# Performance work log

Hardware: AMD Instinct MI355X
Metric: run time of the kernel (lower is better)

## Reference

```python
import jax, jax.numpy as jnp
import numpy as np

NEG_SLOPE = 0.2


def setup_inputs() -> dict:
    key = jax.random.key(0)
    k1, k2, k3, k4, k5, k6 = jax.random.split(key, 6)
    N, E, IN, OUT = 100000, 1600000, 256, 32
    feat = jax.random.normal(k1, (N, IN), dtype=jnp.float32)
    W = jax.random.normal(k2, (IN, OUT), dtype=jnp.float32) * (1.0 / np.sqrt(IN))
    attn_l = jax.random.normal(k3, (OUT,), dtype=jnp.float32) * 0.1
    attn_r = jax.random.normal(k4, (OUT,), dtype=jnp.float32) * 0.1
    bias = jnp.zeros((OUT,), dtype=jnp.float32)
    src = jax.random.randint(k5, (E,), 0, N, dtype=jnp.int32)
    dst = jax.random.randint(k6, (E,), 0, N, dtype=jnp.int32)
    return {"feat": feat, "W": W, "attn_l": attn_l, "attn_r": attn_r,
            "bias": bias, "src": src, "dst": dst}


def reference(feat, W, attn_l, attn_r, bias, src, dst):
    N = feat.shape[0]
    # dense projection: [N, in] @ [in, out] -> [N, out]
    h = feat @ W
    el = h @ attn_l  # [N]
    er = h @ attn_r  # [N]
    # per-edge raw score: el[u] + er[v] for edge u->v
    e = el[src] + er[dst]  # [E]
    e = jnp.where(e > 0, e, NEG_SLOPE * e)  # leaky relu
    # edge softmax grouped by destination node (numerically stable)
    m = jax.ops.segment_max(e, dst, num_segments=N)  # [N], -inf for isolated nodes
    m = jax.lax.stop_gradient(m)
    ex = jnp.exp(e - m[dst])  # [E]
    denom = jax.ops.segment_sum(ex, dst, num_segments=N)  # [N]
    alpha = ex / denom[dst]  # [E]
    # weighted aggregation (sparse SpMM): sum_{u->v} alpha_uv * h[u]
    rst = jax.ops.segment_sum(h[src] * alpha[:, None], dst, num_segments=N)  # [N, out]
    return rst + bias
```

## Files before the change

kernel.cpp:

```cpp
#include <hip/hip_runtime.h>
#include <hip/hip_bf16.h>
#include <math.h>

#define NEG_SLOPE 0.2f
#define BUCK_BITS 5
#define BUCK_NODES 32
#define CAP 800
#define SRC_MASK 0x1FFFFFF
#define NBUK_MAX 3200

#define CBITS 8
#define CNODES 256
#define CAPC 4672
#define NC_MAX 400
#define NBIN 256

typedef __bf16 bf16x8 __attribute__((ext_vector_type(8)));
typedef __bf16 bf16x4 __attribute__((ext_vector_type(4)));
typedef float  f32x4  __attribute__((ext_vector_type(4)));

__global__ void prep(const float* __restrict__ W, __bf16* __restrict__ Whi,
                     unsigned int* __restrict__ fcur,
                     unsigned int* __restrict__ ccur) {
    int idx = blockIdx.x * blockDim.x + threadIdx.x;
    if (idx < NBUK_MAX) fcur[idx] = 0u;
    if (idx < NC_MAX)   ccur[idx] = 0u;
    if (idx >= 8192) return;
    int j = idx & 7, lane = (idx >> 3) & 63, nt = (idx >> 9) & 1, kt = idx >> 10;
    int q = lane >> 4, c = lane & 15;
    int k = kt * 32 + q * 8 + j;
    int n = nt * 16 + c;
    Whi[idx] = (__bf16)W[k * 32 + n];
}

__global__ __launch_bounds__(256) void gemm_bin(const float* __restrict__ feat,
                                                const __bf16* __restrict__ Whi,
                                                const float* __restrict__ attn_l,
                                                const float* __restrict__ attn_r,
                                                const int* __restrict__ src,
                                                const int* __restrict__ dst,
                                                __bf16* __restrict__ hb,
                                                float* __restrict__ el,
                                                float* __restrict__ er,
                                                unsigned int* __restrict__ ccur,
                                                unsigned int* __restrict__ cbin,
                                                int N, int Ntiles, int E, int NC) {
    __shared__ bf16x8 sB[1024];
    int bid = blockIdx.x;
    int tid = threadIdx.x;
    int role, gid;
    if (bid < 2 * NBIN) { role = bid & 1; gid = bid >> 1; }
    else                { role = 0;       gid = bid - NBIN; }

    if (role == 1) {
        unsigned int* hist  = (unsigned int*)sB;
        unsigned int* cbase = hist + NC_MAX;
        int batch = (((E + NBIN - 1) / NBIN) + 3) & ~3;
        int b0 = gid * batch;
        int b1 = min(b0 + batch, E);
        int nv = (b0 < b1) ? ((b1 - b0) >> 2) : 0;
        const int4* d4 = (const int4*)(dst + b0);
        const int4* s4 = (const int4*)(src + b0);
        for (int i = tid; i < NC; i += 256) hist[i] = 0;
        __syncthreads();
        for (int i = tid; i < nv; i += 256) {
            int4 dd = d4[i];
#pragma unroll
            for (int j = 0; j < 4; j++)
                atomicAdd(&hist[((unsigned)(&dd.x)[j]) >> CBITS], 1u);
        }
        __syncthreads();
        for (int i = tid; i < NC; i += 256) {
            unsigned c = hist[i];
            cbase[i] = c ? atomicAdd(&ccur[i], c) : 0u;
            hist[i] = 0;
        }
        __syncthreads();
        for (int i = tid; i < nv; i += 256) {
            int4 dd = d4[i];
            int4 ss = s4[i];
#pragma unroll
            for (int j = 0; j < 4; j++) {
                int d = (&dd.x)[j];
                int s = (&ss.x)[j];
                unsigned cb = ((unsigned)d) >> CBITS;
                unsigned r = atomicAdd(&hist[cb], 1u);
                unsigned pos = cbase[cb] + r;
                if (pos < CAPC)
                    cbin[(size_t)cb * CAPC + pos] =
                        ((unsigned)(d & (CNODES - 1)) << 17) | (unsigned)s;
            }
        }
        return;
    }

    for (int i = tid; i < 1024; i += 256) sB[i] = ((const bf16x8*)Whi)[i];
    __syncthreads();

    int wid  = gid * 4 + (tid >> 6);
    int lane = tid & 63;
    if (wid >= Ntiles) return;

    int c = lane & 15, q = lane >> 4;
    int row = wid * 16 + c;
    if (row >= N) row = N - 1;
    const f32x4* A = (const f32x4*)(feat + (size_t)row * 256 + q * 8);

    f32x4 a[16];
#pragma unroll
    for (int kt = 0; kt < 8; kt++) {
        a[2 * kt]     = A[kt * 8];
        a[2 * kt + 1] = A[kt * 8 + 1];
    }
#pragma unroll
    for (int i = 0; i < 16; i++)
        asm volatile("" : "+v"(a[i]));
    __builtin_amdgcn_sched_barrier(0);

    f32x4 acc0 = {0.f, 0.f, 0.f, 0.f};
    f32x4 acc1 = {0.f, 0.f, 0.f, 0.f};
#pragma unroll
    for (int kt = 0; kt < 8; kt++) {
        f32x4 a0 = a[2 * kt];
        f32x4 a1 = a[2 * kt + 1];
        bf16x8 ah, al;
#pragma unroll
        for (int j = 0; j < 4; j++) {
            __bf16 h0 = (__bf16)a0[j];
            __bf16 h1 = (__bf16)a1[j];
            ah[j]     = h0;
            ah[j + 4] = h1;
            al[j]     = (__bf16)(a0[j] - (float)h0);
            al[j + 4] = (__bf16)(a1[j] - (float)h1);
        }
        bf16x8 bh0 = sB[(kt * 2 + 0) * 64 + lane];
        bf16x8 bh1 = sB[(kt * 2 + 1) * 64 + lane];
        acc0 = __builtin_amdgcn_mfma_f32_16x16x32_bf16(ah, bh0, acc0, 0, 0, 0);
        acc0 = __builtin_amdgcn_mfma_f32_16x16x32_bf16(al, bh0, acc0, 0, 0, 0);
        acc1 = __builtin_amdgcn_mfma_f32_16x16x32_bf16(ah, bh1, acc1, 0, 0, 0);
        acc1 = __builtin_amdgcn_mfma_f32_16x16x32_bf16(al, bh1, acc1, 0, 0, 0);
    }

    float alc  = attn_l[c],      arc  = attn_r[c];
    float alc2 = attn_l[c + 16], arc2 = attn_r[c + 16];
#pragma unroll
    for (int r = 0; r < 4; r++) {
        int m = wid * 16 + q * 4 + r;
        if (m < N) {
            hb[(size_t)m * 32 + c]      = (__bf16)acc0[r];
            hb[(size_t)m * 32 + 16 + c] = (__bf16)acc1[r];
        }
        float pl = acc0[r] * alc + acc1[r] * alc2;
        float pr = acc0[r] * arc + acc1[r] * arc2;
#pragma unroll
        for (int off = 8; off >= 1; off >>= 1) {
            pl += __shfl_xor(pl, off);
            pr += __shfl_xor(pr, off);
        }
        if (c == 0 && m < N) { el[m] = pl; er[m] = pr; }
    }
}

__global__ __launch_bounds__(256) void refine(const unsigned int* __restrict__ ccur,
                                              const unsigned int* __restrict__ cbin,
                                              unsigned int* __restrict__ fcur,
                                              unsigned int* __restrict__ fbin,
                                              int NC) {
    __shared__ unsigned int hist[8];
    __shared__ unsigned int basec[8];
    int blk = blockIdx.x;
    int cb = blk >> 1, seg = blk & 1;
    if (cb >= NC) return;
    int tid = threadIdx.x;
    int cnt = (int)min(ccur[cb], (unsigned)CAPC);
    int lo = (cnt * seg) >> 1;
    int hi = (cnt * (seg + 1)) >> 1;

    if (tid < 8) hist[tid] = 0;
    __syncthreads();
    const unsigned int* cp = cbin + (size_t)cb * CAPC;
    for (int i = lo + tid; i < hi; i += 256)
        atomicAdd(&hist[(cp[i] >> (17 + BUCK_BITS)) & 7], 1u);
    __syncthreads();
    if (tid < 8) {
        unsigned v = hist[tid];
        basec[tid] = v ? atomicAdd(&fcur[cb * 8 + tid], v) : 0u;
        hist[tid] = 0;
    }
    __syncthreads();
    for (int i = lo + tid; i < hi; i += 256) {
        unsigned r = cp[i];
        int fb = (r >> (17 + BUCK_BITS)) & 7;
        unsigned rank = atomicAdd(&hist[fb], 1u);
        unsigned pos = basec[fb] + rank;
        if (pos < CAP)
            fbin[(size_t)(cb * 8 + fb) * CAP + pos] =
                (((r >> 17) & (BUCK_NODES - 1)) << 25) | (r & 0x1FFFFu);
    }
}

__global__ __launch_bounds__(256) void aggregate(const unsigned int* __restrict__ cursor,
                                                 const unsigned int* __restrict__ binned,
                                                 const float* __restrict__ el,
                                                 const float* __restrict__ er,
                                                 const __bf16* __restrict__ hb,
                                                 const float* __restrict__ bias,
                                                 float* __restrict__ out, int N) {
    __shared__ uint2        rw_s[CAP];
    __shared__ unsigned int hist[BUCK_NODES];
    __shared__ int          off_s[BUCK_NODES + 1];
    __shared__ float        den[BUCK_NODES];
    __shared__ float        er_l[BUCK_NODES];

    int buck = blockIdx.x;
    int base = buck << BUCK_BITS;
    int nn = min(BUCK_NODES, N - base);
    int tid = threadIdx.x;

    int cnt = (int)min(cursor[buck], (unsigned)CAP);
    const unsigned int* eb = binned + (size_t)buck * CAP;

    if (tid < BUCK_NODES) {
        hist[tid] = 0;
        den[tid] = 0.f;
        er_l[tid] = (tid < nn) ? er[base + tid] : 0.f;
    }
    __syncthreads();

    unsigned int rl[4];
    int k = 0;
    for (int i = tid; i < cnt; i += 256) {
        unsigned r = eb[i];
        rl[k++] = r;
        atomicAdd(&hist[r >> 25], 1u);
    }
    __syncthreads();

    if (tid < BUCK_NODES) {
        int v = (int)hist[tid];
        int orig = v;
#pragma unroll
        for (int off = 1; off < BUCK_NODES; off <<= 1) {
            int x = __shfl_up(v, off, 64);
            if (tid >= off) v += x;
        }
        off_s[tid] = v - orig;
        if (tid == BUCK_NODES - 1) off_s[BUCK_NODES] = v;
        hist[tid] = (unsigned)(v - orig);
    }
    __syncthreads();

    k = 0;
    for (int i = tid; i < cnt; i += 256) {
        unsigned r = rl[k++];
        int s = r & SRC_MASK;
        int d = r >> 25;
        float e = el[s] + er_l[d];
        e = (e > 0.f) ? e : NEG_SLOPE * e;
        float w = __expf(e);
        unsigned pos = atomicAdd(&hist[d], 1u);
        rw_s[pos] = make_uint2((unsigned)s, __float_as_uint(w));
        atomicAdd(&den[d], w);
    }
    __syncthreads();

    int lane = tid & 63, wv = tid >> 6;
    int oct = lane >> 3, t = lane & 7;
    f32x4 b4 = *(const f32x4*)&bias[t * 4];
    for (int n = wv; n < nn; n += 4) {
        float sm = den[n];
        int s0 = off_s[n], s1 = off_s[n + 1];
        f32x4 acc = {0.f, 0.f, 0.f, 0.f};
#pragma unroll 2
        for (int j = s0 + oct; j < s1; j += 8) {
            uint2 rw = rw_s[j];
            float w = __uint_as_float(rw.y);
            bf16x4 hv = *(const bf16x4*)&hb[(size_t)rw.x * 32 + t * 4];
            acc[0] += w * (float)hv[0];
            acc[1] += w * (float)hv[1];
            acc[2] += w * (float)hv[2];
            acc[3] += w * (float)hv[3];
        }
#pragma unroll
        for (int off = 8; off <= 32; off <<= 1) {
            acc[0] += __shfl_xor(acc[0], off);
            acc[1] += __shfl_xor(acc[1], off);
            acc[2] += __shfl_xor(acc[2], off);
            acc[3] += __shfl_xor(acc[3], off);
        }
        if (lane < 8) {
            f32x4 o;
            if (sm > 0.f) {
                float inv = 1.f / sm;
                o[0] = acc[0] * inv + b4[0];
                o[1] = acc[1] * inv + b4[1];
                o[2] = acc[2] * inv + b4[2];
                o[3] = acc[3] * inv + b4[3];
            } else {
                o = b4;
            }
            *(f32x4*)&out[(size_t)(base + n) * 32 + t * 4] = o;
        }
    }
}

static inline size_t align256(size_t x) { return (x + 255) & ~(size_t)255; }

extern "C" void kernel_launch(void* const* d_in, const int* in_sizes, int n_in,
                              void* d_out, int out_size, void* d_ws, size_t ws_size,
                              hipStream_t stream) {
    const float* feat   = (const float*)d_in[0];
    const float* W      = (const float*)d_in[1];
    const float* attn_l = (const float*)d_in[2];
    const float* attn_r = (const float*)d_in[3];
    const float* bias   = (const float*)d_in[4];
    const int* src = (const int*)d_in[5];
    const int* dst = (const int*)d_in[6];
    float* out = (float*)d_out;

    const int IN = 256;
    int N = in_sizes[0] / IN;
    int E = in_sizes[5];
    (void)n_in; (void)out_size; (void)ws_size;

    int Ntiles = (N + 15) / 16;
    int NBUK = (N + BUCK_NODES - 1) >> BUCK_BITS;
    int NC   = (N + CNODES - 1) >> CBITS;
    int NG   = (Ntiles + 3) / 4;

    char* p = (char*)d_ws;
    __bf16* hb     = (__bf16*)p; p += align256((size_t)N * 32 * 2);
    float* el      = (float*)p; p += align256((size_t)N * 4);
    float* er      = (float*)p; p += align256((size_t)N * 4);
    unsigned int* fcur = (unsigned int*)p; p += align256((size_t)NBUK_MAX * 4);
    unsigned int* ccur = (unsigned int*)p; p += align256((size_t)NC_MAX * 4);
    unsigned int* fbin = (unsigned int*)p; p += align256((size_t)NBUK * CAP * 4);
    unsigned int* cbin = (unsigned int*)p; p += align256((size_t)NC * CAPC * 4);
    __bf16* Whi    = (__bf16*)p; p += align256((size_t)8192 * 2);

    prep<<<33, 256, 0, stream>>>(W, Whi, fcur, ccur);
    gemm_bin<<<NG + NBIN, 256, 0, stream>>>(feat, Whi, attn_l, attn_r, src, dst,
                                            hb, el, er, ccur, cbin,
                                            N, Ntiles, E, NC);
    refine<<<NC * 2, 256, 0, stream>>>(ccur, cbin, fcur, fbin, NC);
    aggregate<<<NBUK, 256, 0, stream>>>(fcur, fbin, el, er, hb, bias, out, N);
}
```

Measured before the change: 249.0 us.

## Make GEMM blocks persistent with double-buffered async global-to-LDS feature staging

Replaces the one-tile-per-wave GEMM launch with 256 persistent GEMM blocks interleaved with the 256 binning blocks. Each wave loops over tiles strided by 1024. Feature rows are streamed into a per-wave double-buffered, XOR-swizzled LDS stage using global_load_lds, with explicit vmcnt waits, so the next quarter-tile loads while the current one runs on MFMA. The aim is to hide the latency of the feature load, which is bound by memory bandwidth. In exchange it uses much more LDS per block (16 KB of weights plus 32 KB of staging), which may lower occupancy. It also relies on the hand-tuned waitcnt being correct.

```diff
diff --git a/kernel.cpp b/kernel.cpp
--- a/kernel.cpp
+++ b/kernel.cpp
@@ -14,6 +14,7 @@
 #define CAPC 4672
 #define NC_MAX 400
 #define NBIN 256
+#define NGEMM 256
 
 typedef __bf16 bf16x8 __attribute__((ext_vector_type(8)));
 typedef __bf16 bf16x4 __attribute__((ext_vector_type(4)));
@@ -45,16 +46,19 @@
                                                 unsigned int* __restrict__ ccur,
                                                 unsigned int* __restrict__ cbin,
                                                 int N, int Ntiles, int E, int NC) {
-    __shared__ bf16x8 sB[1024];
+    union SM {
+        struct { bf16x8 whi[1024]; float stage[4][2][1024]; } g;
+        struct { unsigned int hist[NC_MAX]; unsigned int cbase[NC_MAX]; } b;
+    };
+    __shared__ SM sm;
+
     int bid = blockIdx.x;
     int tid = threadIdx.x;
-    int role, gid;
-    if (bid < 2 * NBIN) { role = bid & 1; gid = bid >> 1; }
-    else                { role = 0;       gid = bid - NBIN; }
+    int role = bid & 1, gid = bid >> 1;
 
     if (role == 1) {
-        unsigned int* hist  = (unsigned int*)sB;
-        unsigned int* cbase = hist + NC_MAX;
+        unsigned int* hist  = sm.b.hist;
+        unsigned int* cbase = sm.b.cbase;
         int batch = (((E + NBIN - 1) / NBIN) + 3) & ~3;
         int b0 = gid * batch;
         int b1 = min(b0 + batch, E);
@@ -94,70 +98,104 @@
         return;
     }
 
-    for (int i = tid; i < 1024; i += 256) sB[i] = ((const bf16x8*)Whi)[i];
-    __syncthreads();
-
-    int wid  = gid * 4 + (tid >> 6);
+    for (int i = tid; i < 1024; i += 256) sm.g.whi[i] = ((const bf16x8*)Whi)[i];
+    __syncthreads();
+
+    int wv   = tid >> 6;
     int lane = tid & 63;
-    if (wid >= Ntiles) return;
-
-    int c = lane & 15, q = lane >> 4;
-    int row = wid * 16 + c;
-    if (row >= N) row = N - 1;
-    const f32x4* A = (const f32x4*)(feat + (size_t)row * 256 + q * 8);
-
-    f32x4 a[16];
-#pragma unroll
-    for (int kt = 0; kt < 8; kt++) {
-        a[2 * kt]     = A[kt * 8];
-        a[2 * kt + 1] = A[kt * 8 + 1];
-    }
-#pragma unroll
-    for (int i = 0; i < 16; i++)
-        asm volatile("" : "+v"(a[i]));
-    __builtin_amdgcn_sched_barrier(0);
+    int cc = lane & 15, qd = lane >> 4;
+    int swz = (cc & 7) << 4;
+
+    int gw = gid * 4 + wv;
+    int nt = (Ntiles - gw + 1023) >> 10;
+    int Q  = 4 * nt;
+
+    float* buf0 = &sm.g.stage[wv][0][0];
+    float* buf1 = &sm.g.stage[wv][1][0];
+
+    auto stage_q = [&](int q) {
+        int qc = q < Q ? q : Q - 1;
+        int t  = gw + ((qc >> 2) << 10);
+        int kq = qc & 3;
+        float* lb = (q & 1) ? buf1 : buf0;
+#pragma unroll
+        for (int j = 0; j < 4; j++) {
+            int r = 4 * j + (lane >> 4);
+            int grow = t * 16 + r;
+            if (grow >= N) grow = N - 1;
+            int seg = ((lane & 15) * 16) ^ ((r & 7) << 4);
+            const char* sp = (const char*)feat +
+                             ((size_t)grow * 256 + kq * 64) * 4 + seg;
+            __builtin_amdgcn_global_load_lds(
+                (const __attribute__((address_space(1))) void*)sp,
+                (__attribute__((address_space(3))) void*)(lb + j * 256),
+                16, 0, 0);
+        }
+    };
+
+    stage_q(0);
+    stage_q(1);
+
+    float alc  = attn_l[cc],      arc  = attn_r[cc];
+    float alc2 = attn_l[cc + 16], arc2 = attn_r[cc + 16];
 
     f32x4 acc0 = {0.f, 0.f, 0.f, 0.f};
     f32x4 acc1 = {0.f, 0.f, 0.f, 0.f};
-#pragma unroll
-    for (int kt = 0; kt < 8; kt++) {
-        f32x4 a0 = a[2 * kt];
-        f32x4 a1 = a[2 * kt + 1];
-        bf16x8 ah, al;
-#pragma unroll
-        for (int j = 0; j < 4; j++) {
-            __bf16 h0 = (__bf16)a0[j];
-            __bf16 h1 = (__bf16)a1[j];
-            ah[j]     = h0;
-            ah[j + 4] = h1;
-            al[j]     = (__bf16)(a0[j] - (float)h0);
-            al[j + 4] = (__bf16)(a1[j] - (float)h1);
-        }
-        bf16x8 bh0 = sB[(kt * 2 + 0) * 64 + lane];
-        bf16x8 bh1 = sB[(kt * 2 + 1) * 64 + lane];
-        acc0 = __builtin_amdgcn_mfma_f32_16x16x32_bf16(ah, bh0, acc0, 0, 0, 0);
-        acc0 = __builtin_amdgcn_mfma_f32_16x16x32_bf16(al, bh0, acc0, 0, 0, 0);
-        acc1 = __builtin_amdgcn_mfma_f32_16x16x32_bf16(ah, bh1, acc1, 0, 0, 0);
-        acc1 = __builtin_amdgcn_mfma_f32_16x16x32_bf16(al, bh1, acc1, 0, 0, 0);
-    }
-
-    float alc  = attn_l[c],      arc  = attn_r[c];
-    float alc2 = attn_l[c + 16], arc2 = attn_r[c + 16];
-#pragma unroll
-    for (int r = 0; r < 4; r++) {
-        int m = wid * 16 + q * 4 + r;
-        if (m < N) {
-            hb[(size_t)m * 32 + c]      = (__bf16)acc0[r];
-            hb[(size_t)m * 32 + 16 + c] = (__bf16)acc1[r];
-        }
-        float pl = acc0[r] * alc + acc1[r] * alc2;
-        float pr = acc0[r] * arc + acc1[r] * arc2;
-#pragma unroll
-        for (int off = 8; off >= 1; off >>= 1) {
-            pl += __shfl_xor(pl, off);
-            pr += __shfl_xor(pr, off);
-        }
-        if (c == 0 && m < N) { el[m] = pl; er[m] = pr; }
+
+    for (int i = 0; i < nt; i++) {
+#pragma unroll
+        for (int kq2 = 0; kq2 < 4; kq2++) {
+            int q = i * 4 + kq2;
+            asm volatile("s_waitcnt vmcnt(4)" ::: "memory");
+            __builtin_amdgcn_sched_barrier(0);
+            const char* lb = (const char*)((q & 1) ? buf1 : buf0);
+#pragma unroll
+            for (int jj = 0; jj < 2; jj++) {
+                int kt = kq2 * 2 + jj;
+                int so = jj * 128 + qd * 32;
+                f32x4 a0 = *(const f32x4*)(lb + cc * 256 + ((so)      ^ swz));
+                f32x4 a1 = *(const f32x4*)(lb + cc * 256 + ((so + 16) ^ swz));
+                bf16x8 ah, al;
+#pragma unroll
+                for (int j = 0; j < 4; j++) {
+                    __bf16 h0 = (__bf16)a0[j];
+                    __bf16 h1 = (__bf16)a1[j];
+                    ah[j]     = h0;
+                    ah[j + 4] = h1;
+                    al[j]     = (__bf16)(a0[j] - (float)h0);
+                    al[j + 4] = (__bf16)(a1[j] - (float)h1);
+                }
+                bf16x8 bh0 = sm.g.whi[(kt * 2 + 0) * 64 + lane];
+                bf16x8 bh1 = sm.g.whi[(kt * 2 + 1) * 64 + lane];
+                acc0 = __builtin_amdgcn_mfma_f32_16x16x32_bf16(ah, bh0, acc0, 0, 0, 0);
+                acc0 = __builtin_amdgcn_mfma_f32_16x16x32_bf16(al, bh0, acc0, 0, 0, 0);
+                acc1 = __builtin_amdgcn_mfma_f32_16x16x32_bf16(ah, bh1, acc1, 0, 0, 0);
+                acc1 = __builtin_amdgcn_mfma_f32_16x16x32_bf16(al, bh1, acc1, 0, 0, 0);
+            }
+            if (kq2 == 3) {
+                int t = gw + (i << 10);
+#pragma unroll
+                for (int r = 0; r < 4; r++) {
+                    int m = t * 16 + qd * 4 + r;
+                    if (m < N) {
+                        hb[(size_t)m * 32 + cc]      = (__bf16)acc0[r];
+                        hb[(size_t)m * 32 + 16 + cc] = (__bf16)acc1[r];
+                    }
+                    float pl = acc0[r] * alc + acc1[r] * alc2;
+                    float pr = acc0[r] * arc + acc1[r] * arc2;
+#pragma unroll
+                    for (int off = 8; off >= 1; off >>= 1) {
+                        pl += __shfl_xor(pl, off);
+                        pr += __shfl_xor(pr, off);
+                    }
+                    if (cc == 0 && m < N) { el[m] = pl; er[m] = pr; }
+                }
+                acc0 = (f32x4){0.f, 0.f, 0.f, 0.f};
+                acc1 = (f32x4){0.f, 0.f, 0.f, 0.f};
+            }
+            __builtin_amdgcn_sched_barrier(0);
+            stage_q(q + 2);
+        }
     }
 }
 
@@ -326,7 +364,6 @@
     int Ntiles = (N + 15) / 16;
     int NBUK = (N + BUCK_NODES - 1) >> BUCK_BITS;
     int NC   = (N + CNODES - 1) >> CBITS;
-    int NG   = (Ntiles + 3) / 4;
 
     char* p = (char*)d_ws;
     __bf16* hb     = (__bf16*)p; p += align256((size_t)N * 32 * 2);
@@ -339,9 +376,9 @@
     __bf16* Whi    = (__bf16*)p; p += align256((size_t)8192 * 2);
 
     prep<<<33, 256, 0, stream>>>(W, Whi, fcur, ccur);
-    gemm_bin<<<NG + NBIN, 256, 0, stream>>>(feat, Whi, attn_l, attn_r, src, dst,
-                                            hb, el, er, ccur, cbin,
-                                            N, Ntiles, E, NC);
+    gemm_bin<<<NGEMM + NBIN, 256, 0, stream>>>(feat, Whi, attn_l, attn_r,
+                                               src, dst, hb, el, er, ccur, cbin,
+                                               N, Ntiles, E, NC);
     refine<<<NC * 2, 256, 0, stream>>>(ccur, cbin, fcur, fbin, NC);
     aggregate<<<NBUK, 256, 0, stream>>>(fcur, fbin, el, er, hb, bias, out, N);
 }
```

Measured after the change: 227.1 us, median of 2. 1.1x faster.
